# Kernel tuning notes

Measured on AMD Instinct MI355X. Metric: run time of the kernel, lower is better.

## Reference

```python
import jax, jax.numpy as jnp
import numpy as np

RATE = 0.1
INPUT_SHAPE = [8192]
BATCH_DIMS = 1
K = max(1, round(RATE * int(np.prod(INPUT_SHAPE))))  # 819


def setup_inputs() -> dict:
    key = jax.random.key(0)
    x = jax.random.normal(key, (4096, 8192), dtype=jnp.float32)
    return {"x": x}


def reference(x) -> jnp.ndarray:
    batch_flat = int(np.prod(x.shape[:BATCH_DIMS]))
    x_flat = x.reshape(batch_flat, -1)            # [B, D]
    ax = jnp.abs(x_flat)
    topk_vals, _ = jax.lax.top_k(ax, K)           # [B, K] sorted descending
    thr = topk_vals[:, -1:]                        # kth largest |x| per row
    mask = (ax >= thr).reshape(x.shape)
    return jnp.where(mask, x, jnp.zeros_like(x))
```

## Files before the change

kernel.cpp:

```cpp
#include <hip/hip_runtime.h>
#include <stdint.h>


constexpr int NCOLS = 8192;
constexpr int TPB   = 256;
constexpr int V4    = NCOLS / 4;
constexpr int VPT   = V4 / TPB;

constexpr int PAD = 8;
constexpr int W1  = 1024;
constexpr int S1  = W1 + PAD;
constexpr int C1  = 2;
constexpr int B2  = 1024;
constexpr int S2  = B2 + PAD;
constexpr int HW  = (C1 * S1 > S2) ? C1 * S1 : S2;

struct Shared {
  uint32_t hist[HW];
  uint32_t wavesum[4];
  uint32_t digit;
  uint32_t rem;
};

template <int BPT>
__device__ __forceinline__ uint32_t pick_winner(Shared& sh, const uint32_t (&hb)[BPT],
                                                uint32_t& rem, int tid, int lane, int wave) {
  uint32_t L = 0;
#pragma unroll
  for (int j = 0; j < BPT; ++j) L += hb[j];

  uint32_t suf = L;
#pragma unroll
  for (int off = 1; off < 64; off <<= 1) {
    uint32_t o = __shfl_down(suf, off, 64);
    suf += (lane + off < 64) ? o : 0u;
  }
  if (lane == 0) sh.wavesum[wave] = suf;
  __syncthreads();
  uint32_t addw = 0;
#pragma unroll
  for (int w = 0; w < 4; ++w) addw += (w > wave) ? sh.wavesum[w] : 0u;
  suf += addw;

  uint32_t s = suf - L;
#pragma unroll
  for (int j = BPT - 1; j >= 0; --j) {
    uint32_t snext = s;
    s += hb[j];
    if (s >= rem && snext < rem) {
      sh.digit = (uint32_t)(tid * BPT + j);
      sh.rem = rem - snext;
    }
  }
  __syncthreads();
  uint32_t d = sh.digit;
  rem = sh.rem;
  return d;
}

__device__ __forceinline__ uint32_t phase1(Shared& sh, const uint4 (&v)[VPT],
                                           uint32_t& rem, int tid, int lane, int wave) {
  uint4* hz = (uint4*)sh.hist;
  constexpr int ZW4 = (C1 * S1) / 4;
  for (int i = tid; i < ZW4; i += TPB) hz[i] = make_uint4(0u, 0u, 0u, 0u);
  __syncthreads();

  uint32_t* h = &sh.hist[(wave >> 1) * S1];
#pragma unroll
  for (int i = 0; i < VPT; ++i) {
    uint32_t a[4] = {v[i].x, v[i].y, v[i].z, v[i].w};
#pragma unroll
    for (int j = 0; j < 4; ++j) {
      uint32_t d = (a[j] & 0x7fffffffu) >> 20;
      atomicAdd(&h[d & (W1 - 1)], 1u << ((d >> 10) << 4));
    }
  }
  __syncthreads();

  constexpr int BPT = 2048 / TPB;
  uint32_t hb[BPT];
#pragma unroll
  for (int j = 0; j < BPT; ++j) hb[j] = 0;
  const int wbase = (tid & 127) * BPT;
  const int shift = (tid >> 7) << 4;
#pragma unroll
  for (int c = 0; c < C1; ++c) {
    const uint4* hp = (const uint4*)&sh.hist[c * S1 + wbase];
#pragma unroll
    for (int q = 0; q < BPT / 4; ++q) {
      uint4 t = hp[q];
      hb[4 * q + 0] += (t.x >> shift) & 0xffffu;
      hb[4 * q + 1] += (t.y >> shift) & 0xffffu;
      hb[4 * q + 2] += (t.z >> shift) & 0xffffu;
      hb[4 * q + 3] += (t.w >> shift) & 0xffffu;
    }
  }
  return pick_winner<BPT>(sh, hb, rem, tid, lane, wave);
}

__device__ __forceinline__ uint32_t phase23(Shared& sh, const uint4 (&v)[VPT],
                                            int dshift, int cshift, uint32_t cprefix,
                                            uint32_t& rem, int tid, int lane, int wave) {
  uint4* hz = (uint4*)sh.hist;
  constexpr int ZW4 = S2 / 4;
  for (int i = tid; i < ZW4; i += TPB) hz[i] = make_uint4(0u, 0u, 0u, 0u);
  __syncthreads();

#pragma unroll
  for (int i = 0; i < VPT; ++i) {
    uint32_t a[4] = {v[i].x, v[i].y, v[i].z, v[i].w};
#pragma unroll
    for (int j = 0; j < 4; ++j) {
      uint32_t key = a[j] & 0x7fffffffu;
      if ((key >> cshift) == cprefix)
        atomicAdd(&sh.hist[(key >> dshift) & (B2 - 1)], 1u);
    }
  }
  __syncthreads();

  constexpr int BPT = B2 / TPB;
  uint32_t hb[BPT];
  const uint4 t = *(const uint4*)&sh.hist[tid * BPT];
  hb[0] = t.x; hb[1] = t.y; hb[2] = t.z; hb[3] = t.w;
  return pick_winner<BPT>(sh, hb, rem, tid, lane, wave);
}

__global__ __launch_bounds__(TPB, 4) void topk_row_kernel(const float* __restrict__ x,
                                                          float* __restrict__ out,
                                                          int K) {
  __shared__ Shared sh;
  const int row  = blockIdx.x;
  const int tid  = threadIdx.x;
  const int lane = tid & 63;
  const int wave = tid >> 6;

  const uint4* xr = (const uint4*)(x) + (size_t)row * V4;
  uint4 v[VPT];
#pragma unroll
  for (int i = 0; i < VPT; ++i) v[i] = xr[tid + i * TPB];

#pragma unroll
  for (int i = 0; i < VPT; ++i)
    asm volatile("" : "+v"(v[i].x), "+v"(v[i].y), "+v"(v[i].z), "+v"(v[i].w));

  uint32_t rem = (uint32_t)K;
  uint32_t d1 = phase1(sh, v, rem, tid, lane, wave);
  uint32_t d2 = phase23(sh, v, 10, 20, d1, rem, tid, lane, wave);
  uint32_t d3 = phase23(sh, v,  0, 10, (d1 << 10) | d2, rem, tid, lane, wave);

  const uint32_t thr = (d1 << 20) | (d2 << 10) | d3;

  uint4* outr = (uint4*)(out) + (size_t)row * V4;
#pragma unroll
  for (int i = 0; i < VPT; ++i) {
    uint4 o = v[i];
    o.x = ((o.x & 0x7fffffffu) >= thr) ? o.x : 0u;
    o.y = ((o.y & 0x7fffffffu) >= thr) ? o.y : 0u;
    o.z = ((o.z & 0x7fffffffu) >= thr) ? o.z : 0u;
    o.w = ((o.w & 0x7fffffffu) >= thr) ? o.w : 0u;
    outr[tid + i * TPB] = o;
  }
}

extern "C" void kernel_launch(void* const* d_in, const int* in_sizes, int n_in,
                              void* d_out, int out_size, void* d_ws, size_t ws_size,
                              hipStream_t stream) {
  (void)n_in; (void)out_size; (void)d_ws; (void)ws_size;
  const float* x = (const float*)d_in[0];
  float* out = (float*)d_out;
  const int rows = in_sizes[0] / NCOLS;
  const int K = (int)(0.1 * NCOLS + 0.5);
  topk_row_kernel<<<rows, TPB, 0, stream>>>(x, out, K);
}
```

Measured before the change: 229.6 us.

## Process two rows per block with interleaved radix-select histograms

Each block now handles two rows at once, holding both rows' values in registers and interleaving the histogram atomics, prefix scans and digit selection for the pair. Both rows share every barrier and scan, which halves the number of synchronisations per row and gives more independent work to hide LDS atomic latency. In exchange, each thread doubles its register footprint (64 extra VGPRs for values), LDS use roughly doubles, and the grid is halved. That may lower occupancy and reduce memory-level parallelism across blocks.

Measured after the change: 235.6 us. 2.6% more time.

```diff
diff --git a/kernel.cpp b/kernel.cpp
--- a/kernel.cpp
+++ b/kernel.cpp
@@ -6,159 +6,219 @@
 constexpr int TPB   = 256;
 constexpr int V4    = NCOLS / 4;
 constexpr int VPT   = V4 / TPB;
+constexpr int RPB   = 2;
 
 constexpr int PAD = 8;
 constexpr int W1  = 1024;
 constexpr int S1  = W1 + PAD;
-constexpr int C1  = 2;
 constexpr int B2  = 1024;
 constexpr int S2  = B2 + PAD;
-constexpr int HW  = (C1 * S1 > S2) ? C1 * S1 : S2;
+constexpr int HW  = 4 * S1;
 
 struct Shared {
   uint32_t hist[HW];
-  uint32_t wavesum[4];
-  uint32_t digit;
-  uint32_t rem;
+  uint32_t wavesumA[4], wavesumB[4];
+  uint32_t digitA, remA, digitB, remB;
 };
 
 template <int BPT>
-__device__ __forceinline__ uint32_t pick_winner(Shared& sh, const uint32_t (&hb)[BPT],
-                                                uint32_t& rem, int tid, int lane, int wave) {
-  uint32_t L = 0;
-#pragma unroll
-  for (int j = 0; j < BPT; ++j) L += hb[j];
-
-  uint32_t suf = L;
+__device__ __forceinline__ void pick_pair(Shared& sh,
+                                          const uint32_t (&hbA)[BPT],
+                                          const uint32_t (&hbB)[BPT],
+                                          uint32_t& remA, uint32_t& remB,
+                                          uint32_t& dA, uint32_t& dB,
+                                          int tid, int lane, int wave) {
+  uint32_t LA = 0, LB = 0;
+#pragma unroll
+  for (int j = 0; j < BPT; ++j) { LA += hbA[j]; LB += hbB[j]; }
+
+  uint32_t sufA = LA, sufB = LB;
 #pragma unroll
   for (int off = 1; off < 64; off <<= 1) {
-    uint32_t o = __shfl_down(suf, off, 64);
-    suf += (lane + off < 64) ? o : 0u;
-  }
-  if (lane == 0) sh.wavesum[wave] = suf;
-  __syncthreads();
-  uint32_t addw = 0;
-#pragma unroll
-  for (int w = 0; w < 4; ++w) addw += (w > wave) ? sh.wavesum[w] : 0u;
-  suf += addw;
-
-  uint32_t s = suf - L;
+    uint32_t oA = __shfl_down(sufA, off, 64);
+    uint32_t oB = __shfl_down(sufB, off, 64);
+    sufA += (lane + off < 64) ? oA : 0u;
+    sufB += (lane + off < 64) ? oB : 0u;
+  }
+  if (lane == 0) { sh.wavesumA[wave] = sufA; sh.wavesumB[wave] = sufB; }
+  __syncthreads();
+  uint32_t addwA = 0, addwB = 0;
+#pragma unroll
+  for (int w = 0; w < 4; ++w) {
+    addwA += (w > wave) ? sh.wavesumA[w] : 0u;
+    addwB += (w > wave) ? sh.wavesumB[w] : 0u;
+  }
+  sufA += addwA; sufB += addwB;
+
+  uint32_t sA = sufA - LA;
 #pragma unroll
   for (int j = BPT - 1; j >= 0; --j) {
-    uint32_t snext = s;
-    s += hb[j];
-    if (s >= rem && snext < rem) {
-      sh.digit = (uint32_t)(tid * BPT + j);
-      sh.rem = rem - snext;
-    }
-  }
-  __syncthreads();
-  uint32_t d = sh.digit;
-  rem = sh.rem;
-  return d;
-}
-
-__device__ __forceinline__ uint32_t phase1(Shared& sh, const uint4 (&v)[VPT],
-                                           uint32_t& rem, int tid, int lane, int wave) {
+    uint32_t snext = sA;
+    sA += hbA[j];
+    if (sA >= remA && snext < remA) {
+      sh.digitA = (uint32_t)(tid * BPT + j);
+      sh.remA = remA - snext;
+    }
+  }
+  uint32_t sB = sufB - LB;
+#pragma unroll
+  for (int j = BPT - 1; j >= 0; --j) {
+    uint32_t snext = sB;
+    sB += hbB[j];
+    if (sB >= remB && snext < remB) {
+      sh.digitB = (uint32_t)(tid * BPT + j);
+      sh.remB = remB - snext;
+    }
+  }
+  __syncthreads();
+  dA = sh.digitA; remA = sh.remA;
+  dB = sh.digitB; remB = sh.remB;
+}
+
+__device__ __forceinline__ void phase1_pair(Shared& sh,
+                                            const uint4 (&vA)[VPT],
+                                            const uint4 (&vB)[VPT],
+                                            uint32_t& remA, uint32_t& remB,
+                                            uint32_t& d1A, uint32_t& d1B,
+                                            int tid, int lane, int wave) {
   uint4* hz = (uint4*)sh.hist;
-  constexpr int ZW4 = (C1 * S1) / 4;
+  constexpr int ZW4 = (4 * S1) / 4;
   for (int i = tid; i < ZW4; i += TPB) hz[i] = make_uint4(0u, 0u, 0u, 0u);
   __syncthreads();
 
-  uint32_t* h = &sh.hist[(wave >> 1) * S1];
-#pragma unroll
-  for (int i = 0; i < VPT; ++i) {
-    uint32_t a[4] = {v[i].x, v[i].y, v[i].z, v[i].w};
+  uint32_t* hA = &sh.hist[(wave >> 1) * S1];
+  uint32_t* hB = &sh.hist[(2 + (wave >> 1)) * S1];
+#pragma unroll
+  for (int i = 0; i < VPT; ++i) {
+    uint32_t aA[4] = {vA[i].x, vA[i].y, vA[i].z, vA[i].w};
+    uint32_t aB[4] = {vB[i].x, vB[i].y, vB[i].z, vB[i].w};
 #pragma unroll
     for (int j = 0; j < 4; ++j) {
-      uint32_t d = (a[j] & 0x7fffffffu) >> 20;
-      atomicAdd(&h[d & (W1 - 1)], 1u << ((d >> 10) << 4));
+      uint32_t dA = (aA[j] & 0x7fffffffu) >> 20;
+      uint32_t dB = (aB[j] & 0x7fffffffu) >> 20;
+      atomicAdd(&hA[dA & (W1 - 1)], 1u << ((dA >> 10) << 4));
+      atomicAdd(&hB[dB & (W1 - 1)], 1u << ((dB >> 10) << 4));
     }
   }
   __syncthreads();
 
   constexpr int BPT = 2048 / TPB;
-  uint32_t hb[BPT];
-#pragma unroll
-  for (int j = 0; j < BPT; ++j) hb[j] = 0;
+  uint32_t hbA[BPT], hbB[BPT];
+#pragma unroll
+  for (int j = 0; j < BPT; ++j) { hbA[j] = 0; hbB[j] = 0; }
   const int wbase = (tid & 127) * BPT;
   const int shift = (tid >> 7) << 4;
 #pragma unroll
-  for (int c = 0; c < C1; ++c) {
-    const uint4* hp = (const uint4*)&sh.hist[c * S1 + wbase];
+  for (int c = 0; c < 2; ++c) {
+    const uint4* hpA = (const uint4*)&sh.hist[c * S1 + wbase];
+    const uint4* hpB = (const uint4*)&sh.hist[(2 + c) * S1 + wbase];
 #pragma unroll
     for (int q = 0; q < BPT / 4; ++q) {
-      uint4 t = hp[q];
-      hb[4 * q + 0] += (t.x >> shift) & 0xffffu;
-      hb[4 * q + 1] += (t.y >> shift) & 0xffffu;
-      hb[4 * q + 2] += (t.z >> shift) & 0xffffu;
-      hb[4 * q + 3] += (t.w >> shift) & 0xffffu;
-    }
-  }
-  return pick_winner<BPT>(sh, hb, rem, tid, lane, wave);
-}
-
-__device__ __forceinline__ uint32_t phase23(Shared& sh, const uint4 (&v)[VPT],
-                                            int dshift, int cshift, uint32_t cprefix,
-                                            uint32_t& rem, int tid, int lane, int wave) {
+      uint4 tA = hpA[q], tB = hpB[q];
+      hbA[4 * q + 0] += (tA.x >> shift) & 0xffffu;
+      hbA[4 * q + 1] += (tA.y >> shift) & 0xffffu;
+      hbA[4 * q + 2] += (tA.z >> shift) & 0xffffu;
+      hbA[4 * q + 3] += (tA.w >> shift) & 0xffffu;
+      hbB[4 * q + 0] += (tB.x >> shift) & 0xffffu;
+      hbB[4 * q + 1] += (tB.y >> shift) & 0xffffu;
+      hbB[4 * q + 2] += (tB.z >> shift) & 0xffffu;
+      hbB[4 * q + 3] += (tB.w >> shift) & 0xffffu;
+    }
+  }
+  pick_pair<BPT>(sh, hbA, hbB, remA, remB, d1A, d1B, tid, lane, wave);
+}
+
+__device__ __forceinline__ void phase23_pair(Shared& sh,
+                                             const uint4 (&vA)[VPT],
+                                             const uint4 (&vB)[VPT],
+                                             int dshift, int cshift,
+                                             uint32_t prefA, uint32_t prefB,
+                                             uint32_t& remA, uint32_t& remB,
+                                             uint32_t& dA, uint32_t& dB,
+                                             int tid, int lane, int wave) {
   uint4* hz = (uint4*)sh.hist;
-  constexpr int ZW4 = S2 / 4;
+  constexpr int ZW4 = (2 * S2) / 4;
   for (int i = tid; i < ZW4; i += TPB) hz[i] = make_uint4(0u, 0u, 0u, 0u);
   __syncthreads();
 
 #pragma unroll
   for (int i = 0; i < VPT; ++i) {
-    uint32_t a[4] = {v[i].x, v[i].y, v[i].z, v[i].w};
+    uint32_t aA[4] = {vA[i].x, vA[i].y, vA[i].z, vA[i].w};
+    uint32_t aB[4] = {vB[i].x, vB[i].y, vB[i].z, vB[i].w};
 #pragma unroll
     for (int j = 0; j < 4; ++j) {
-      uint32_t key = a[j] & 0x7fffffffu;
-      if ((key >> cshift) == cprefix)
-        atomicAdd(&sh.hist[(key >> dshift) & (B2 - 1)], 1u);
+      uint32_t kA = aA[j] & 0x7fffffffu;
+      uint32_t kB = aB[j] & 0x7fffffffu;
+      if ((kA >> cshift) == prefA)
+        atomicAdd(&sh.hist[(kA >> dshift) & (B2 - 1)], 1u);
+      if ((kB >> cshift) == prefB)
+        atomicAdd(&sh.hist[S2 + ((kB >> dshift) & (B2 - 1))], 1u);
     }
   }
   __syncthreads();
 
   constexpr int BPT = B2 / TPB;
-  uint32_t hb[BPT];
-  const uint4 t = *(const uint4*)&sh.hist[tid * BPT];
-  hb[0] = t.x; hb[1] = t.y; hb[2] = t.z; hb[3] = t.w;
-  return pick_winner<BPT>(sh, hb, rem, tid, lane, wave);
+  uint32_t hbA[BPT], hbB[BPT];
+  const uint4 tA = *(const uint4*)&sh.hist[tid * BPT];
+  const uint4 tB = *(const uint4*)&sh.hist[S2 + tid * BPT];
+  hbA[0] = tA.x; hbA[1] = tA.y; hbA[2] = tA.z; hbA[3] = tA.w;
+  hbB[0] = tB.x; hbB[1] = tB.y; hbB[2] = tB.z; hbB[3] = tB.w;
+  pick_pair<BPT>(sh, hbA, hbB, remA, remB, dA, dB, tid, lane, wave);
 }
 
 __global__ __launch_bounds__(TPB, 4) void topk_row_kernel(const float* __restrict__ x,
                                                           float* __restrict__ out,
-                                                          int K) {
+                                                          int K, int nrows) {
   __shared__ Shared sh;
-  const int row  = blockIdx.x;
   const int tid  = threadIdx.x;
   const int lane = tid & 63;
   const int wave = tid >> 6;
-
-  const uint4* xr = (const uint4*)(x) + (size_t)row * V4;
-  uint4 v[VPT];
-#pragma unroll
-  for (int i = 0; i < VPT; ++i) v[i] = xr[tid + i * TPB];
-
-#pragma unroll
-  for (int i = 0; i < VPT; ++i)
-    asm volatile("" : "+v"(v[i].x), "+v"(v[i].y), "+v"(v[i].z), "+v"(v[i].w));
-
-  uint32_t rem = (uint32_t)K;
-  uint32_t d1 = phase1(sh, v, rem, tid, lane, wave);
-  uint32_t d2 = phase23(sh, v, 10, 20, d1, rem, tid, lane, wave);
-  uint32_t d3 = phase23(sh, v,  0, 10, (d1 << 10) | d2, rem, tid, lane, wave);
-
-  const uint32_t thr = (d1 << 20) | (d2 << 10) | d3;
-
-  uint4* outr = (uint4*)(out) + (size_t)row * V4;
-#pragma unroll
-  for (int i = 0; i < VPT; ++i) {
-    uint4 o = v[i];
-    o.x = ((o.x & 0x7fffffffu) >= thr) ? o.x : 0u;
-    o.y = ((o.y & 0x7fffffffu) >= thr) ? o.y : 0u;
-    o.z = ((o.z & 0x7fffffffu) >= thr) ? o.z : 0u;
-    o.w = ((o.w & 0x7fffffffu) >= thr) ? o.w : 0u;
-    outr[tid + i * TPB] = o;
+  const int rowA = blockIdx.x * RPB;
+  const bool hasB = (rowA + 1 < nrows);
+
+  const uint4* xrA = (const uint4*)(x) + (size_t)rowA * V4;
+  const uint4* xrB = hasB ? (xrA + V4) : xrA;
+
+  uint4 vA[VPT], vB[VPT];
+#pragma unroll
+  for (int i = 0; i < VPT; ++i) { vA[i] = xrA[tid + i * TPB]; vB[i] = xrB[tid + i * TPB]; }
+#pragma unroll
+  for (int i = 0; i < VPT; ++i) {
+    asm volatile("" : "+v"(vA[i].x), "+v"(vA[i].y), "+v"(vA[i].z), "+v"(vA[i].w));
+    asm volatile("" : "+v"(vB[i].x), "+v"(vB[i].y), "+v"(vB[i].z), "+v"(vB[i].w));
+  }
+
+  uint32_t remA = (uint32_t)K, remB = (uint32_t)K;
+  uint32_t d1A, d1B, d2A, d2B, d3A, d3B;
+  phase1_pair(sh, vA, vB, remA, remB, d1A, d1B, tid, lane, wave);
+  phase23_pair(sh, vA, vB, 10, 20, d1A, d1B, remA, remB, d2A, d2B, tid, lane, wave);
+  phase23_pair(sh, vA, vB, 0, 10, (d1A << 10) | d2A, (d1B << 10) | d2B,
+               remA, remB, d3A, d3B, tid, lane, wave);
+
+  const uint32_t thrA = (d1A << 20) | (d2A << 10) | d3A;
+  const uint32_t thrB = (d1B << 20) | (d2B << 10) | d3B;
+
+  uint4* outA = (uint4*)(out) + (size_t)rowA * V4;
+#pragma unroll
+  for (int i = 0; i < VPT; ++i) {
+    uint4 o = vA[i];
+    o.x = ((o.x & 0x7fffffffu) >= thrA) ? o.x : 0u;
+    o.y = ((o.y & 0x7fffffffu) >= thrA) ? o.y : 0u;
+    o.z = ((o.z & 0x7fffffffu) >= thrA) ? o.z : 0u;
+    o.w = ((o.w & 0x7fffffffu) >= thrA) ? o.w : 0u;
+    outA[tid + i * TPB] = o;
+  }
+  if (hasB) {
+    uint4* outB = outA + V4;
+#pragma unroll
+    for (int i = 0; i < VPT; ++i) {
+      uint4 o = vB[i];
+      o.x = ((o.x & 0x7fffffffu) >= thrB) ? o.x : 0u;
+      o.y = ((o.y & 0x7fffffffu) >= thrB) ? o.y : 0u;
+      o.z = ((o.z & 0x7fffffffu) >= thrB) ? o.z : 0u;
+      o.w = ((o.w & 0x7fffffffu) >= thrB) ? o.w : 0u;
+      outB[tid + i * TPB] = o;
+    }
   }
 }
 
@@ -170,5 +230,6 @@
   float* out = (float*)d_out;
   const int rows = in_sizes[0] / NCOLS;
   const int K = (int)(0.1 * NCOLS + 0.5);
-  topk_row_kernel<<<rows, TPB, 0, stream>>>(x, out, K);
-}
+  const int grid = (rows + RPB - 1) / RPB;
+  topk_row_kernel<<<grid, TPB, 0, stream>>>(x, out, K, rows);
+}
```

## Compact top-digit candidates into LDS list for later radix passes

Applied to the files above, without the earlier changes.

After the first radix histogram picks the top 11-bit digit, elements matching that digit are appended to a shared-memory candidate list via an atomic counter. The second and third radix passes then histogram only this short list instead of rescanning all register-held values per thread. A fallback to the full scan is kept when the list overflows. This adds a per-candidate LDS atomic and 8KB of extra shared memory, which may reduce occupancy.

Result: no change. 233.4 us (+1.7%).

```diff
diff --git a/kernel.cpp b/kernel.cpp
--- a/kernel.cpp
+++ b/kernel.cpp
@@ -15,11 +15,15 @@
 constexpr int S2  = B2 + PAD;
 constexpr int HW  = (C1 * S1 > S2) ? C1 * S1 : S2;
 
+constexpr int CAND_MAX = 2048;
+
 struct Shared {
   uint32_t hist[HW];
+  uint32_t cand[CAND_MAX];
   uint32_t wavesum[4];
   uint32_t digit;
   uint32_t rem;
+  uint32_t cnt;
 };
 
 template <int BPT>
@@ -63,6 +67,7 @@
   uint4* hz = (uint4*)sh.hist;
   constexpr int ZW4 = (C1 * S1) / 4;
   for (int i = tid; i < ZW4; i += TPB) hz[i] = make_uint4(0u, 0u, 0u, 0u);
+  if (tid == 0) sh.cnt = 0;
   __syncthreads();
 
   uint32_t* h = &sh.hist[(wave >> 1) * S1];
@@ -98,9 +103,32 @@
   return pick_winner<BPT>(sh, hb, rem, tid, lane, wave);
 }
 
-__device__ __forceinline__ uint32_t phase23(Shared& sh, const uint4 (&v)[VPT],
-                                            int dshift, int cshift, uint32_t cprefix,
-                                            uint32_t& rem, int tid, int lane, int wave) {
+template <bool FILTER>
+__device__ __forceinline__ uint32_t phase_list(Shared& sh, int dshift,
+                                               uint32_t d2match, uint32_t total,
+                                               uint32_t& rem, int tid, int lane, int wave) {
+  uint4* hz = (uint4*)sh.hist;
+  constexpr int ZW4 = S2 / 4;
+  for (int i = tid; i < ZW4; i += TPB) hz[i] = make_uint4(0u, 0u, 0u, 0u);
+  __syncthreads();
+
+  for (uint32_t p = tid; p < total; p += TPB) {
+    uint32_t key = sh.cand[p];
+    if (!FILTER || (((key >> 10) & 1023u) == d2match))
+      atomicAdd(&sh.hist[(key >> dshift) & (B2 - 1)], 1u);
+  }
+  __syncthreads();
+
+  constexpr int BPT = B2 / TPB;
+  uint32_t hb[BPT];
+  const uint4 t = *(const uint4*)&sh.hist[tid * BPT];
+  hb[0] = t.x; hb[1] = t.y; hb[2] = t.z; hb[3] = t.w;
+  return pick_winner<BPT>(sh, hb, rem, tid, lane, wave);
+}
+
+__device__ __forceinline__ uint32_t phase23_full(Shared& sh, const uint4 (&v)[VPT],
+                                                 int dshift, int cshift, uint32_t cprefix,
+                                                 uint32_t& rem, int tid, int lane, int wave) {
   uint4* hz = (uint4*)sh.hist;
   constexpr int ZW4 = S2 / 4;
   for (int i = tid; i < ZW4; i += TPB) hz[i] = make_uint4(0u, 0u, 0u, 0u);
@@ -145,8 +173,30 @@
 
   uint32_t rem = (uint32_t)K;
   uint32_t d1 = phase1(sh, v, rem, tid, lane, wave);
-  uint32_t d2 = phase23(sh, v, 10, 20, d1, rem, tid, lane, wave);
-  uint32_t d3 = phase23(sh, v,  0, 10, (d1 << 10) | d2, rem, tid, lane, wave);
+
+#pragma unroll
+  for (int i = 0; i < VPT; ++i) {
+    uint32_t a[4] = {v[i].x, v[i].y, v[i].z, v[i].w};
+#pragma unroll
+    for (int j = 0; j < 4; ++j) {
+      uint32_t key = a[j] & 0x7fffffffu;
+      if ((key >> 20) == d1) {
+        uint32_t p = atomicAdd(&sh.cnt, 1u);
+        if (p < (uint32_t)CAND_MAX) sh.cand[p] = key;
+      }
+    }
+  }
+  __syncthreads();
+  const uint32_t total = sh.cnt;
+
+  uint32_t d2, d3;
+  if (total <= (uint32_t)CAND_MAX) {
+    d2 = phase_list<false>(sh, 10, 0, total, rem, tid, lane, wave);
+    d3 = phase_list<true>(sh, 0, d2, total, rem, tid, lane, wave);
+  } else {
+    d2 = phase23_full(sh, v, 10, 20, d1, rem, tid, lane, wave);
+    d3 = phase23_full(sh, v, 0, 10, (d1 << 10) | d2, rem, tid, lane, wave);
+  }
 
   const uint32_t thr = (d1 << 20) | (d2 << 10) | d3;
 
```
